# Kernel tuning notes

Hardware: AMD Instinct MI355X
Metric: run time of the kernel (lower is better)

Reference implementation:

```python
import jax, jax.numpy as jnp
import numpy as np

B, T, C, H = 2, 2048, 1024, 16
HS = C // H

def setup_inputs() -> dict:
    key = jax.random.key(0)
    ks = jax.random.split(key, 5)
    s = 0.02
    return {
        "x": jax.random.normal(ks[0], (B, T, C), jnp.float32),
        "W_attn": jax.random.normal(ks[1], (C, 3 * C), jnp.float32) * s,
        "b_attn": jax.random.normal(ks[2], (3 * C,), jnp.float32) * s,
        "W_proj": jax.random.normal(ks[3], (C, C), jnp.float32) * s,
        "b_proj": jax.random.normal(ks[4], (C,), jnp.float32) * s,
    }

def reference(x, W_attn, b_attn, W_proj, b_proj):
    qkv = x @ W_attn + b_attn                      # [B,T,3C]
    q, k, v = jnp.split(qkv, 3, axis=-1)
    # [B,T,C] -> [B,H,T,hs]
    def heads(t):
        return t.reshape(B, T, H, HS).transpose(0, 2, 1, 3)
    q, k, v = heads(q), heads(k), heads(v)
    scale = 1.0 / jnp.sqrt(jnp.asarray(HS, x.dtype))
    attn = jnp.einsum('bhqd,bhkd->bhqk', q, k) * scale
    causal = jnp.tril(jnp.ones((T, T), bool))
    attn = jnp.where(causal[None, None], attn, -jnp.inf)
    attn = jax.nn.softmax(attn, axis=-1)
    y = jnp.einsum('bhqk,bhkd->bhqd', attn, v)
    y = y.transpose(0, 2, 1, 3).reshape(B, T, C)
    return y @ W_proj + b_proj
```

## Files before the change

### kernel.cpp

```cpp
#include <hip/hip_runtime.h>
#include <hip/hip_bf16.h>

static constexpr int Bn = 2, Tn = 2048, Cn = 1024, Hn = 16, HSn = 64;
static constexpr int Mrows = Bn * Tn;
static constexpr size_t PL = (size_t)Bn * Hn * Tn * HSn;

typedef __attribute__((ext_vector_type(8))) short short8;
typedef __attribute__((ext_vector_type(4))) float f32x4;

__device__ __forceinline__ unsigned short f2bf(float f) {
  __hip_bfloat16 h = __float2bfloat16(f);
  return *reinterpret_cast<unsigned short*>(&h);
}

__device__ __forceinline__ float fexp2(float x) {
  return __builtin_amdgcn_exp2f(x);
}

__device__ __forceinline__ void gload_lds16(const void* g, void* l) {
  __builtin_amdgcn_global_load_lds(
      (const __attribute__((address_space(1))) void*)g,
      (__attribute__((address_space(3))) void*)l, 16, 0, 0);
}

#define QSC 0.18033688011112042591999058512524f

__global__ __launch_bounds__(256) void prep_all(
    const float* __restrict__ x, unsigned short* __restrict__ xb,
    const float* __restrict__ Wa, unsigned short* __restrict__ Wab,
    const float* __restrict__ Wp, unsigned short* __restrict__ Wpb)
{
  const int bid = blockIdx.x, tid = threadIdx.x;
  if (bid < 4096) {
    int i = bid * 256 + tid;
    float4 v = ((const float4*)x)[i];
    ushort4 o;
    o.x = f2bf(v.x); o.y = f2bf(v.y); o.z = f2bf(v.z); o.w = f2bf(v.w);
    ((ushort4*)xb)[i] = o;
    return;
  }
  __shared__ float tile[32][33];
  const float* src; unsigned short* dst; int R, Cc, tb;
  if (bid < 4096 + 3072) { src = Wa; dst = Wab; R = Cn; Cc = 3 * Cn; tb = bid - 4096; }
  else                   { src = Wp; dst = Wpb; R = Cn; Cc = Cn;     tb = bid - 4096 - 3072; }
  const int nbx = Cc / 32;
  const int bx = tb % nbx, by = tb / nbx;
  const int tx = tid & 31, ty = tid >> 5;
  const int c0 = bx * 32, r0 = by * 32;
  #pragma unroll
  for (int i = 0; i < 4; ++i)
    tile[ty + 8 * i][tx] = src[(size_t)(r0 + ty + 8 * i) * Cc + c0 + tx];
  __syncthreads();
  #pragma unroll
  for (int i = 0; i < 4; ++i)
    dst[(size_t)(c0 + ty + 8 * i) * R + r0 + tx] = f2bf(tile[tx][ty + 8 * i]);
}

__global__ __launch_bounds__(512) void gemmQKV(
    const unsigned short* __restrict__ A, const unsigned short* __restrict__ Bt,
    const float* __restrict__ bias, unsigned short* __restrict__ qkv, int K)
{
  constexpr int NSTEP = 1024 / 64;
  constexpr int AF = 32;
  constexpr int BF = 24;
  __shared__ alignas(16) unsigned char lds[2][(AF + BF) * 1024];

  const int tid = threadIdx.x, wave = tid >> 6, lane = tid & 63;
  const int wr = wave >> 2, wc = wave & 3;
  const int orig = blockIdx.x;
  const int swz = (orig & 7) * 32 + (orig >> 3);
  const int bx = swz & 15, by = swz >> 4;
  const int tM = by * 256, tN = bx * 192;

  auto STAGE = [&](int buf, int k0) {
    #pragma unroll
    for (int i = 0; i < 7; ++i) {
      int f = wave * 7 + i;
      const unsigned short* g;
      int off;
      if (f < AF) {
        int mg = f >> 1, ks = f & 1;
        g = A + (size_t)(tM + mg * 16 + (lane & 15)) * K + k0 + ks * 32 + (lane >> 4) * 8;
        off = f * 1024;
      } else {
        int fg = f - AF;
        int ng = fg >> 1, ks = fg & 1;
        g = Bt + (size_t)(tN + ng * 16 + (lane & 15)) * K + k0 + ks * 32 + (lane >> 4) * 8;
        off = AF * 1024 + fg * 1024;
      }
      gload_lds16(g, &lds[buf][off]);
    }
  };

  f32x4 acc[8][3] = {};

  STAGE(0, 0);
  STAGE(1, 64);

  for (int t = 0; t < NSTEP; ++t) {
    if (t == NSTEP - 1)
      asm volatile("s_waitcnt vmcnt(0)" ::: "memory");
    else
      asm volatile("s_waitcnt vmcnt(7)" ::: "memory");
    __builtin_amdgcn_s_barrier();

    const int cur = t & 1;
    short8 af[8][2], bfr[3][2];
    #pragma unroll
    for (int ks = 0; ks < 2; ++ks) {
      #pragma unroll
      for (int m = 0; m < 8; ++m)
        af[m][ks] = *(const short8*)&lds[cur][((wr * 8 + m) * 2 + ks) * 1024 + lane * 16];
      #pragma unroll
      for (int n = 0; n < 3; ++n)
        bfr[n][ks] = *(const short8*)&lds[cur][AF * 1024 + ((wc * 3 + n) * 2 + ks) * 1024 + lane * 16];
    }
    asm volatile("s_waitcnt lgkmcnt(0)" ::: "memory");
    __builtin_amdgcn_sched_barrier(0);
    __builtin_amdgcn_s_barrier();

    if (t + 2 < NSTEP) STAGE(cur, (t + 2) * 64);

    __builtin_amdgcn_s_setprio(1);
    #pragma unroll
    for (int ks = 0; ks < 2; ++ks)
      #pragma unroll
      for (int m = 0; m < 8; ++m)
        #pragma unroll
        for (int n = 0; n < 3; ++n)
          acc[m][n] = __builtin_amdgcn_mfma_f32_16x16x32_bf16(af[m][ks], bfr[n][ks], acc[m][n], 0, 0, 0);
    __builtin_amdgcn_s_setprio(0);
  }

  const int a = lane & 15, hq = lane >> 4;
  #pragma unroll
  for (int m = 0; m < 8; ++m) {
    #pragma unroll
    for (int n = 0; n < 3; ++n) {
      int c = tN + wc * 48 + n * 16 + a;
      float bv = bias[c];
      int which = c >> 10;
      int cc = c & 1023, hh = cc >> 6, d = cc & 63;
      int row0 = tM + wr * 128 + m * 16 + hq * 4;
      int b = row0 >> 11, t0 = row0 & 2047;
      int bh = b * Hn + hh;
      if (which == 2) {
        ushort4 pk;
        pk.x = f2bf(acc[m][n][0] + bv);
        pk.y = f2bf(acc[m][n][1] + bv);
        pk.z = f2bf(acc[m][n][2] + bv);
        pk.w = f2bf(acc[m][n][3] + bv);
        *(ushort4*)&qkv[2 * PL + ((size_t)bh * HSn + d) * Tn + t0] = pk;
      } else {
        float sc = (which == 0) ? QSC : 1.0f;
        #pragma unroll
        for (int r = 0; r < 4; ++r) {
          float v = (acc[m][n][r] + bv) * sc;
          qkv[(size_t)which * PL + ((size_t)bh * Tn + t0 + r) * HSn + d] = f2bf(v);
        }
      }
    }
  }
}

template <int WM, int WN>
__global__ __launch_bounds__(256) void gemmP(
    const unsigned short* __restrict__ A, const unsigned short* __restrict__ Bt,
    const float* __restrict__ bias, float* __restrict__ O, int N, int K)
{
  constexpr int BM = WM * 32, BNt = WN * 32;
  constexpr int AF = BM / 16;
  constexpr int BF = BNt / 16;
  constexpr int NF = AF + BF;
  constexpr int PW = NF / 4;
  static_assert(PW == 3, "vmcnt literal");
  __shared__ alignas(16) unsigned char lds[2][NF * 1024];

  const int tid = threadIdx.x, wave = tid >> 6, lane = tid & 63;
  const int wr = wave >> 1, wc = wave & 1;
  const int orig = blockIdx.x;
  const int swz = (orig & 7) * 64 + (orig >> 3);
  const int bx = swz & 15, by = swz >> 4;
  const int tM = by * BM, tN = bx * BNt;

  auto STAGE = [&](int buf, int k0) {
    #pragma unroll
    for (int i = 0; i < PW; ++i) {
      int f = wave * PW + i;
      const unsigned short* g;
      if (f < AF)
        g = A + (size_t)(tM + f * 16 + (lane & 15)) * K + k0 + (lane >> 4) * 8;
      else
        g = Bt + (size_t)(tN + (f - AF) * 16 + (lane & 15)) * K + k0 + (lane >> 4) * 8;
      gload_lds16(g, &lds[buf][f * 1024]);
    }
  };

  f32x4 acc[WM][WN] = {};

  STAGE(0, 0);
  for (int t = 0, k0 = 0;; ++t, k0 += 32) {
    const int cur = t & 1;
    if (k0 + 32 < K) {
      STAGE(cur ^ 1, k0 + 32);
      asm volatile("s_waitcnt vmcnt(3)" ::: "memory");
    } else {
      asm volatile("s_waitcnt vmcnt(0)" ::: "memory");
    }
    __builtin_amdgcn_s_barrier();

    short8 af[WM], bfr[WN];
    #pragma unroll
    for (int m = 0; m < WM; ++m)
      af[m] = *(const short8*)&lds[cur][(wr * WM + m) * 1024 + lane * 16];
    #pragma unroll
    for (int n = 0; n < WN; ++n)
      bfr[n] = *(const short8*)&lds[cur][(AF + wc * WN + n) * 1024 + lane * 16];
    #pragma unroll
    for (int m = 0; m < WM; ++m)
      #pragma unroll
      for (int n = 0; n < WN; ++n)
        acc[m][n] = __builtin_amdgcn_mfma_f32_16x16x32_bf16(af[m], bfr[n], acc[m][n], 0, 0, 0);

    __builtin_amdgcn_s_barrier();
    if (k0 + 32 >= K) break;
  }

  const int a = lane & 15, hq = lane >> 4;
  #pragma unroll
  for (int m = 0; m < WM; ++m) {
    #pragma unroll
    for (int n = 0; n < WN; ++n) {
      int c = tN + wc * (WN * 16) + n * 16 + a;
      float bv = bias[c];
      int r0 = tM + wr * (WM * 16) + m * 16 + hq * 4;
      #pragma unroll
      for (int r = 0; r < 4; ++r)
        O[(size_t)(r0 + r) * N + c] = acc[m][n][r] + bv;
    }
  }
}

__global__ __launch_bounds__(256) void attn_mfma(
    const unsigned short* __restrict__ Qg, const unsigned short* __restrict__ Kg,
    const unsigned short* __restrict__ Vtg, unsigned short* __restrict__ Y)
{
  __shared__ alignas(16) unsigned char lds[50176];
  const int flat = blockIdx.x;
  const int logical = (flat & 7) * 64 + (flat >> 3);
  const int bh = logical >> 4;
  const int yb = logical & 15;
  const int tid = threadIdx.x, wave = tid >> 6, lane = tid & 63;
  const int a = lane & 15, h = lane >> 4;
  const unsigned short* Qp = Qg + (size_t)bh * Tn * HSn;
  const unsigned short* Kp = Kg + (size_t)bh * Tn * HSn;
  const unsigned short* Vp = Vtg + (size_t)bh * HSn * Tn;
  const int pbase = 40960 + wave * 2304;
  const int qglob = wave * 16 + a;
  const int b = bh >> 4, hd = bh & 15;

  auto STAGE_K = [&](int kb, int kv0) {
    #pragma unroll
    for (int i = 0; i < 2; ++i) {
      int r8 = wave * 16 + i * 8;
      int row = r8 + (lane >> 3);
      int ch = (lane & 7) ^ (row & 7);
      gload_lds16(Kp + (size_t)(kv0 + row) * HSn + ch * 8,
                  &lds[8192 + kb * 8192 + r8 * 128]);
    }
  };
  auto STAGE_V = [&](int vb, int kv0) {
    #pragma unroll
    for (int i = 0; i < 2; ++i) {
      int r8 = wave * 16 + i * 8;
      int row = r8 + (lane >> 3);
      int ch = (lane & 7) ^ (row & 7);
      gload_lds16(Vp + (size_t)row * Tn + kv0 + ch * 8,
                  &lds[24576 + vb * 8192 + r8 * 128]);
    }
  };

  short8 ones;
  #pragma unroll
  for (int j = 0; j < 8; ++j) ones[j] = (short)0x3F80;

  for (int ph = 0; ph < 2; ++ph) {
    const int qt = ph ? (31 - yb) : yb;
    const int q0 = qt * 64;

    #pragma unroll
    for (int i = 0; i < 2; ++i) {
      int r8 = wave * 16 + i * 8;
      int row = r8 + (lane >> 3);
      int ch = (lane & 7) ^ (row & 7);
      gload_lds16(Qp + (size_t)(q0 + row) * HSn + ch * 8, &lds[r8 * 128]);
    }
    STAGE_K(0, 0);
    STAGE_V(0, 0);
    if (qt >= 1) {
      STAGE_K(1, 64);
      STAGE_V(1, 64);
      asm volatile("s_waitcnt vmcnt(8)" ::: "memory");
    } else {
      asm volatile("s_waitcnt vmcnt(4)" ::: "memory");
    }

    short8 qf[2];
    #pragma unroll
    for (int ks = 0; ks < 2; ++ks) {
      int row = wave * 16 + a;
      int ch = (ks * 4 + h) ^ (row & 7);
      qf[ks] = *(const short8*)&lds[row * 128 + ch * 16];
    }

    f32x4 o[4] = {};
    f32x4 lacc = {};

    for (int t = 0; t <= qt; ++t) {
      const int kb = t & 1;
      if (t == qt)
        asm volatile("s_waitcnt vmcnt(0)" ::: "memory");
      else
        asm volatile("s_waitcnt vmcnt(4)" ::: "memory");
      __builtin_amdgcn_s_barrier();

      const int kbase = 8192 + kb * 8192;
      const int vbase = 24576 + kb * 8192;

      f32x4 s[4] = {};
      __builtin_amdgcn_s_setprio(1);
      #pragma unroll
      for (int ks = 0; ks < 2; ++ks)
        #pragma unroll
        for (int n = 0; n < 4; ++n) {
          int kr = n * 16 + a;
          int ch = (ks * 4 + h) ^ (kr & 7);
          short8 kf = *(const short8*)&lds[kbase + kr * 128 + ch * 16];
          s[n] = __builtin_amdgcn_mfma_f32_16x16x32_bf16(kf, qf[ks], s[n], 0, 0, 0);
        }
      __builtin_amdgcn_s_setprio(0);

      if (t == qt) {
        #pragma unroll
        for (int n = 0; n < 4; ++n)
          #pragma unroll
          for (int r = 0; r < 4; ++r)
            if ((n * 16 + h * 4 + r) > qglob) s[n][r] = -1e30f;
      }

      #pragma unroll
      for (int n = 0; n < 4; ++n)
        #pragma unroll
        for (int r = 0; r < 4; ++r) s[n][r] = fexp2(s[n][r]);

      #pragma unroll
      for (int n = 0; n < 4; ++n) {
        uint2 w2;
        w2.x = (unsigned)f2bf(s[n][0]) | ((unsigned)f2bf(s[n][1]) << 16);
        w2.y = (unsigned)f2bf(s[n][2]) | ((unsigned)f2bf(s[n][3]) << 16);
        *(uint2*)&lds[pbase + (a * 36 + n * 8 + h * 2) * 4] = w2;
      }

      __builtin_amdgcn_s_setprio(1);
      #pragma unroll
      for (int ks = 0; ks < 2; ++ks) {
        short8 pa = *(const short8*)&lds[pbase + (a * 36 + ks * 16 + h * 4) * 4];
        lacc = __builtin_amdgcn_mfma_f32_16x16x32_bf16(pa, ones, lacc, 0, 0, 0);
        #pragma unroll
        for (int n = 0; n < 4; ++n) {
          int d = n * 16 + a;
          int ch = (ks * 4 + h) ^ (d & 7);
          short8 vf = *(const short8*)&lds[vbase + d * 128 + ch * 16];
          o[n] = __builtin_amdgcn_mfma_f32_16x16x32_bf16(pa, vf, o[n], 0, 0, 0);
        }
      }
      __builtin_amdgcn_s_setprio(0);

      __builtin_amdgcn_s_barrier();
      if (t + 2 <= qt) {
        STAGE_K(kb, (t + 2) * 64);
        STAGE_V(kb, (t + 2) * 64);
      }
    }

    f32x4 inv;
    #pragma unroll
    for (int r = 0; r < 4; ++r) inv[r] = 1.0f / lacc[r];
    #pragma unroll
    for (int n = 0; n < 4; ++n)
      #pragma unroll
      for (int r = 0; r < 4; ++r) {
        int tr = q0 + wave * 16 + 4 * h + r;
        int col = hd * 64 + n * 16 + a;
        Y[((size_t)(b * Tn + tr)) * Cn + col] = f2bf(o[n][r] * inv[r]);
      }
  }
}

extern "C" void kernel_launch(void* const* d_in, const int* in_sizes, int n_in,
                              void* d_out, int out_size, void* d_ws, size_t ws_size,
                              hipStream_t stream) {
  const float* x      = (const float*)d_in[0];
  const float* W_attn = (const float*)d_in[1];
  const float* b_attn = (const float*)d_in[2];
  const float* W_proj = (const float*)d_in[3];
  const float* b_proj = (const float*)d_in[4];
  float* out = (float*)d_out;

  unsigned short* xb  = (unsigned short*)d_ws;
  unsigned short* Wab = xb + (size_t)Mrows * Cn;
  unsigned short* Wpb = Wab + (size_t)3 * Cn * Cn;
  unsigned short* qkv = Wpb + (size_t)Cn * Cn;
  unsigned short* y   = qkv + 3 * PL;

  prep_all<<<4096 + 3072 + 1024, 256, 0, stream>>>(x, xb, W_attn, Wab, W_proj, Wpb);

  gemmQKV<<<256, 512, 0, stream>>>(xb, Wab, b_attn, qkv, Cn);

  attn_mfma<<<512, 256, 0, stream>>>(qkv, qkv + PL, qkv + 2 * PL, y);

  gemmP<4, 2><<<512, 256, 0, stream>>>(y, Wpb, b_proj, out, Cn, Cn);
}
```

Before: 108.6 us.

## Widen attention KV tile to 128 keys with doubled LDS staging buffers

```diff
diff --git a/kernel.cpp b/kernel.cpp
--- a/kernel.cpp
+++ b/kernel.cpp
@@ -245,38 +245,39 @@
     const unsigned short* __restrict__ Qg, const unsigned short* __restrict__ Kg,
     const unsigned short* __restrict__ Vtg, unsigned short* __restrict__ Y)
 {
-  __shared__ alignas(16) unsigned char lds[50176];
+  __shared__ alignas(16) unsigned char lds[74752];
   const int flat = blockIdx.x;
   const int logical = (flat & 7) * 64 + (flat >> 3);
   const int bh = logical >> 4;
   const int yb = logical & 15;
   const int tid = threadIdx.x, wave = tid >> 6, lane = tid & 63;
   const int a = lane & 15, h = lane >> 4;
+  const int a7 = a & 7;
   const unsigned short* Qp = Qg + (size_t)bh * Tn * HSn;
   const unsigned short* Kp = Kg + (size_t)bh * Tn * HSn;
   const unsigned short* Vp = Vtg + (size_t)bh * HSn * Tn;
-  const int pbase = 40960 + wave * 2304;
+  const int pbase = wave * 2304;
   const int qglob = wave * 16 + a;
   const int b = bh >> 4, hd = bh & 15;
 
   auto STAGE_K = [&](int kb, int kv0) {
     #pragma unroll
-    for (int i = 0; i < 2; ++i) {
-      int r8 = wave * 16 + i * 8;
+    for (int i = 0; i < 4; ++i) {
+      int r8 = wave * 32 + i * 8;
       int row = r8 + (lane >> 3);
       int ch = (lane & 7) ^ (row & 7);
       gload_lds16(Kp + (size_t)(kv0 + row) * HSn + ch * 8,
-                  &lds[8192 + kb * 8192 + r8 * 128]);
+                  &lds[9216 + kb * 16384 + r8 * 128]);
     }
   };
   auto STAGE_V = [&](int vb, int kv0) {
     #pragma unroll
-    for (int i = 0; i < 2; ++i) {
-      int r8 = wave * 16 + i * 8;
-      int row = r8 + (lane >> 3);
-      int ch = (lane & 7) ^ (row & 7);
-      gload_lds16(Vp + (size_t)row * Tn + kv0 + ch * 8,
-                  &lds[24576 + vb * 8192 + r8 * 128]);
+    for (int i = 0; i < 4; ++i) {
+      int d4 = wave * 16 + i * 4;
+      int d = d4 + (lane >> 4);
+      int ch = (lane & 15) ^ (d & 7);
+      gload_lds16(Vp + (size_t)d * Tn + kv0 + ch * 8,
+                  &lds[41984 + vb * 16384 + d4 * 256]);
     }
   };
 
@@ -287,6 +288,7 @@
   for (int ph = 0; ph < 2; ++ph) {
     const int qt = ph ? (31 - yb) : yb;
     const int q0 = qt * 64;
+    const int T128 = (qt >> 1) + 1;
 
     #pragma unroll
     for (int i = 0; i < 2; ++i) {
@@ -297,12 +299,12 @@
     }
     STAGE_K(0, 0);
     STAGE_V(0, 0);
-    if (qt >= 1) {
-      STAGE_K(1, 64);
-      STAGE_V(1, 64);
+    if (T128 >= 2) {
+      STAGE_K(1, 128);
+      STAGE_V(1, 128);
+      asm volatile("s_waitcnt vmcnt(16)" ::: "memory");
+    } else {
       asm volatile("s_waitcnt vmcnt(8)" ::: "memory");
-    } else {
-      asm volatile("s_waitcnt vmcnt(4)" ::: "memory");
     }
 
     short8 qf[2];
@@ -316,70 +318,74 @@
     f32x4 o[4] = {};
     f32x4 lacc = {};
 
-    for (int t = 0; t <= qt; ++t) {
+    for (int t = 0; t < T128; ++t) {
       const int kb = t & 1;
-      if (t == qt)
+      const int kv0 = t * 128;
+      if (t == T128 - 1)
         asm volatile("s_waitcnt vmcnt(0)" ::: "memory");
       else
-        asm volatile("s_waitcnt vmcnt(4)" ::: "memory");
+        asm volatile("s_waitcnt vmcnt(8)" ::: "memory");
       __builtin_amdgcn_s_barrier();
 
-      const int kbase = 8192 + kb * 8192;
-      const int vbase = 24576 + kb * 8192;
-
-      f32x4 s[4] = {};
+      const int kbase = 9216 + kb * 16384;
+      const int vbase = 41984 + kb * 16384;
+
+      f32x4 s[8] = {};
       __builtin_amdgcn_s_setprio(1);
       #pragma unroll
       for (int ks = 0; ks < 2; ++ks)
         #pragma unroll
-        for (int n = 0; n < 4; ++n) {
+        for (int n = 0; n < 8; ++n) {
           int kr = n * 16 + a;
-          int ch = (ks * 4 + h) ^ (kr & 7);
+          int ch = (ks * 4 + h) ^ a7;
           short8 kf = *(const short8*)&lds[kbase + kr * 128 + ch * 16];
           s[n] = __builtin_amdgcn_mfma_f32_16x16x32_bf16(kf, qf[ks], s[n], 0, 0, 0);
         }
       __builtin_amdgcn_s_setprio(0);
 
-      if (t == qt) {
-        #pragma unroll
-        for (int n = 0; n < 4; ++n)
+      if (t == T128 - 1) {
+        #pragma unroll
+        for (int n = 0; n < 8; ++n)
           #pragma unroll
           for (int r = 0; r < 4; ++r)
-            if ((n * 16 + h * 4 + r) > qglob) s[n][r] = -1e30f;
-      }
-
-      #pragma unroll
-      for (int n = 0; n < 4; ++n)
+            if ((kv0 + n * 16 + h * 4 + r) > (q0 + qglob)) s[n][r] = -1e30f;
+      }
+
+      #pragma unroll
+      for (int n = 0; n < 8; ++n)
         #pragma unroll
         for (int r = 0; r < 4; ++r) s[n][r] = fexp2(s[n][r]);
 
       #pragma unroll
-      for (int n = 0; n < 4; ++n) {
-        uint2 w2;
-        w2.x = (unsigned)f2bf(s[n][0]) | ((unsigned)f2bf(s[n][1]) << 16);
-        w2.y = (unsigned)f2bf(s[n][2]) | ((unsigned)f2bf(s[n][3]) << 16);
-        *(uint2*)&lds[pbase + (a * 36 + n * 8 + h * 2) * 4] = w2;
-      }
-
-      __builtin_amdgcn_s_setprio(1);
-      #pragma unroll
-      for (int ks = 0; ks < 2; ++ks) {
-        short8 pa = *(const short8*)&lds[pbase + (a * 36 + ks * 16 + h * 4) * 4];
-        lacc = __builtin_amdgcn_mfma_f32_16x16x32_bf16(pa, ones, lacc, 0, 0, 0);
-        #pragma unroll
-        for (int n = 0; n < 4; ++n) {
-          int d = n * 16 + a;
-          int ch = (ks * 4 + h) ^ (d & 7);
-          short8 vf = *(const short8*)&lds[vbase + d * 128 + ch * 16];
-          o[n] = __builtin_amdgcn_mfma_f32_16x16x32_bf16(pa, vf, o[n], 0, 0, 0);
+      for (int hp = 0; hp < 2; ++hp) {
+        #pragma unroll
+        for (int nn = 0; nn < 4; ++nn) {
+          int n = hp * 4 + nn;
+          uint2 w2;
+          w2.x = (unsigned)f2bf(s[n][0]) | ((unsigned)f2bf(s[n][1]) << 16);
+          w2.y = (unsigned)f2bf(s[n][2]) | ((unsigned)f2bf(s[n][3]) << 16);
+          *(uint2*)&lds[pbase + (a * 36 + nn * 8 + h * 2) * 4] = w2;
         }
-      }
-      __builtin_amdgcn_s_setprio(0);
+        __builtin_amdgcn_s_setprio(1);
+        #pragma unroll
+        for (int ks = 0; ks < 2; ++ks) {
+          short8 pa = *(const short8*)&lds[pbase + (a * 36 + ks * 16 + h * 4) * 4];
+          lacc = __builtin_amdgcn_mfma_f32_16x16x32_bf16(pa, ones, lacc, 0, 0, 0);
+          #pragma unroll
+          for (int n = 0; n < 4; ++n) {
+            int d = n * 16 + a;
+            int ch = (hp * 8 + ks * 4 + h) ^ a7;
+            short8 vf = *(const short8*)&lds[vbase + d * 256 + ch * 16];
+            o[n] = __builtin_amdgcn_mfma_f32_16x16x32_bf16(pa, vf, o[n], 0, 0, 0);
+          }
+        }
+        __builtin_amdgcn_s_setprio(0);
+      }
 
       __builtin_amdgcn_s_barrier();
-      if (t + 2 <= qt) {
-        STAGE_K(kb, (t + 2) * 64);
-        STAGE_V(kb, (t + 2) * 64);
+      if (t + 2 < T128) {
+        STAGE_K(kb, (t + 2) * 128);
+        STAGE_V(kb, (t + 2) * 128);
       }
     }
 
```

After: 112.5 us. 3.5% more time.
